# Kernel tuning notes

Measured on AMD Instinct MI355X. Metric: run time of the kernel, lower is better.

Reference implementation:

```python
import jax, jax.numpy as jnp
import numpy as np
from jax import lax

BN_EPS = 1e-5


def _conv(x, w):
    # stride-1, VALID conv; the torch 'locally connected' layer shares weights
    # across pixels, so it is exactly a standard conv2d.
    return lax.conv_general_dilated(
        x, w, window_strides=(1, 1), padding='VALID',
        dimension_numbers=('NCHW', 'OIHW', 'NCHW'))


def _batchnorm(x, gamma, beta):
    # training-mode BatchNorm2d: batch statistics over (N, H, W)
    mean = jnp.mean(x, axis=(0, 2, 3), keepdims=True)
    var = jnp.var(x, axis=(0, 2, 3), keepdims=True)
    xhat = (x - mean) * lax.rsqrt(var + BN_EPS)
    return xhat * gamma[None, :, None, None] + beta[None, :, None, None]


def setup_inputs() -> dict:
    key = jax.random.key(0)
    ks = jax.random.split(key, 6)
    B = 16384
    x = jax.random.normal(ks[0], (B, 256), dtype=jnp.float32)
    w1 = jax.random.normal(ks[1], (16, 1, 3, 3), dtype=jnp.float32)
    w2 = jax.random.normal(ks[2], (32, 16, 2, 2), dtype=jnp.float32)
    w3 = jax.random.normal(ks[3], (64, 32, 1, 1), dtype=jnp.float32)
    fan_in = 64 * 13 * 13
    bound = 1.0 / np.sqrt(fan_in)
    fc_w = jax.random.uniform(ks[4], (10, fan_in), minval=-bound, maxval=bound, dtype=jnp.float32)
    fc_b = jax.random.uniform(ks[5], (10,), minval=-bound, maxval=bound, dtype=jnp.float32)
    return {
        'x': x, 'w1': w1, 'w2': w2, 'w3': w3,
        'g1': jnp.ones((16,), jnp.float32), 'b1': jnp.zeros((16,), jnp.float32),
        'g2': jnp.ones((32,), jnp.float32), 'b2': jnp.zeros((32,), jnp.float32),
        'g3': jnp.ones((64,), jnp.float32), 'b3': jnp.zeros((64,), jnp.float32),
        'fc_w': fc_w, 'fc_b': fc_b,
    }


def reference(x, w1, w2, w3, g1, b1, g2, b2, g3, b3, fc_w, fc_b):
    h = x.reshape(-1, 1, 16, 16)                     # [B,1,16,16]
    h = jax.nn.relu(_batchnorm(_conv(h, w1), g1, b1))  # [B,16,14,14]
    h = jax.nn.relu(_batchnorm(_conv(h, w2), g2, b2))  # [B,32,13,13]
    h = jax.nn.relu(_batchnorm(_conv(h, w3), g3, b3))  # [B,64,13,13]
    h = h.reshape(h.shape[0], -1)                    # [B, 64*13*13]
    # dropout is identity in eval/deterministic mode
    return h @ fc_w.T + fc_b                         # [B,10]
```

## Files before the change

### kernel.cpp

```cpp
#include <hip/hip_runtime.h>


#define NPART 1024
#define P2_OFF 32768
#define ST_OFF 229376
#define ST1 ST_OFF
#define ST2 (ST_OFF + 32)
#define ST3 (ST_OFF + 96)
#define C2R_OFF 230400
#define C1R_OFF 231424
#define C2P_OFF 262144
#define A2G_BYTE 5242880ull
#define FCB_N (13 * 8192)
#define A1S 24
#define A1B 384
#define A3P 1048

typedef __attribute__((ext_vector_type(8))) short bf16x8;
typedef __attribute__((ext_vector_type(4))) float f32x4;

__device__ __forceinline__ unsigned int f2bf(float f) {
  unsigned int u = __float_as_uint(f);
  return (u + 0x7fffu + ((u >> 16) & 1u)) >> 16;
}
__device__ __forceinline__ unsigned int pkbf(float a, float b) {
  unsigned ua = __float_as_uint(a) + 0x8000u;
  unsigned ub = __float_as_uint(b) + 0x8000u;
  return __builtin_amdgcn_perm(ub, ua, 0x07060302u);
}
__device__ __forceinline__ short cvtbf(float a) {
  return (short)((__float_as_uint(a) + 0x8000u) >> 16);
}

__device__ __forceinline__ void conv1_mfma(
    const float* __restrict__ sxi,
    short* ph_buf,
    int r, int b, int q, bf16x8 a1f, f32x4 c1i)
{
  bf16x8 bf = {0, 0, 0, 0, 0, 0, 0, 0};
  unsigned* bu = (unsigned*)&bf;
  if (q == 0) {
    bu[0] = pkbf(sxi[r * 16 + b],           sxi[r * 16 + b + 1]);
    bu[1] = pkbf(sxi[r * 16 + b + 2],       sxi[(r + 1) * 16 + b]);
    bu[2] = pkbf(sxi[(r + 1) * 16 + b + 1], sxi[(r + 1) * 16 + b + 2]);
    bu[3] = pkbf(sxi[(r + 2) * 16 + b],     sxi[(r + 2) * 16 + b + 1]);
  } else if (q == 1) {
    bu[0] = pkbf(sxi[(r + 2) * 16 + b + 2], 0.f);
  }
  f32x4 acc = c1i;
  acc = __builtin_amdgcn_mfma_f32_16x16x32_bf16(a1f, bf, acc, 0, 0, 0);
  float v0 = acc[0] > 0.f ? acc[0] : 0.f;
  float v1 = acc[1] > 0.f ? acc[1] : 0.f;
  float v2 = acc[2] > 0.f ? acc[2] : 0.f;
  float v3 = acc[3] > 0.f ? acc[3] : 0.f;
  uint2 pk;
  pk.x = pkbf(v0, v1);
  pk.y = pkbf(v2, v3);
  *(uint2*)(ph_buf + (r & 1) * A1B + b * A1S + 4 * q) = pk;
}

__device__ __forceinline__ bf16x8 conv1_afrag(const float* w1, float rs1b,
                                              int b, int q) {
  bf16x8 v;
#pragma unroll
  for (int j = 0; j < 8; ++j) {
    int tap = 8 * q + j;
    v[j] = (tap < 9) ? (short)f2bf(w1[b * 9 + tap] * rs1b) : (short)0;
  }
  return v;
}

__global__ __launch_bounds__(256) void k1_xsyrk(
    const float* __restrict__ x, float* __restrict__ parts)
{
  __shared__ float sx[16 * 256];
  const int tid = threadIdx.x, w = tid >> 6, lane = tid & 63;
  const int b = lane & 15, q = lane >> 4;
  {
    const float4* xs = (const float4*)(x + (size_t)blockIdx.x * (16 * 256));
    float4* sd = (float4*)sx;
    for (int e = tid; e < 16 * 64; e += 256) sd[e] = xs[e];
  }
  __syncthreads();
  const int di = (b < 9) ? (b / 3) : 0;
  const int dj = (b < 9) ? (b - di * 3) : 0;
  const int h = q >> 1, jb = (q & 1) * 8;
  f32x4 acc = {0.f, 0.f, 0.f, 0.f};
#pragma unroll 1
  for (int t = 0; t < 4; ++t) {
    const float* sxi = sx + (w * 4 + t) * 256;
#pragma unroll 1
    for (int s = 0; s < 7; ++s) {
      bf16x8 af;
      unsigned* au = (unsigned*)&af;
      if (b < 9) {
        const float* srow = sxi + (2 * s + h + di) * 16 + dj;
#pragma unroll
        for (int cc = 0; cc < 4; ++cc) {
          float v0 = (jb + 2 * cc     < 14) ? srow[jb + 2 * cc]     : 0.f;
          float v1 = (jb + 2 * cc + 1 < 14) ? srow[jb + 2 * cc + 1] : 0.f;
          au[cc] = pkbf(v0, v1);
        }
      } else if (b == 9) {
#pragma unroll
        for (int cc = 0; cc < 4; ++cc) {
          unsigned lo = (jb + 2 * cc     < 14) ? 0x3F80u : 0u;
          unsigned hi = (jb + 2 * cc + 1 < 14) ? 0x3F800000u : 0u;
          au[cc] = lo | hi;
        }
      } else {
#pragma unroll
        for (int cc = 0; cc < 4; ++cc) au[cc] = 0u;
      }
      acc = __builtin_amdgcn_mfma_f32_16x16x32_bf16(af, af, acc, 0, 0, 0);
    }
  }
  __syncthreads();
  float* redc = sx;
#pragma unroll
  for (int rr = 0; rr < 4; ++rr)
    redc[w * 256 + (4 * q + rr) * 16 + b] = acc[rr];
  __syncthreads();
  parts[blockIdx.x * 256 + tid] =
      redc[tid] + redc[256 + tid] + redc[512 + tid] + redc[768 + tid];
}

__global__ __launch_bounds__(256) void k_stats1a(
    const float* __restrict__ parts, float* __restrict__ ws)
{
  const int e = blockIdx.x, tid = threadIdx.x;
  const int w = tid >> 6, lane = tid & 63;
  __shared__ float rs[4];
  float s = 0.f;
#pragma unroll 4
  for (int i = tid; i < 1024; i += 256) s += parts[i * 256 + e];
#pragma unroll
  for (int d = 1; d < 64; d <<= 1) s += __shfl_xor(s, d);
  if (lane == 0) rs[w] = s;
  __syncthreads();
  if (tid == 0) ws[C1R_OFF + e] = rs[0] + rs[1] + rs[2] + rs[3];
}

__global__ __launch_bounds__(64) void k_stats1b(
    const float* __restrict__ w1, const float* __restrict__ gamma,
    const float* __restrict__ beta, float* __restrict__ ws)
{
  const int c = threadIdx.x;
  if (c >= 16) return;
  const float* C = ws + C1R_OFF;
  float wr[9];
#pragma unroll
  for (int p = 0; p < 9; ++p) wr[p] = w1[c * 9 + p];
  float msum = 0.f;
#pragma unroll
  for (int p = 0; p < 9; ++p) msum += wr[p] * C[9 * 16 + p];
  float e2 = 0.f;
#pragma unroll
  for (int a = 0; a < 9; ++a)
#pragma unroll
    for (int bb = 0; bb < 9; ++bb)
      e2 += wr[a] * wr[bb] * C[a * 16 + bb];
  const float inv_n = 1.0f / (16384.0f * 196.0f);
  float mean = msum * inv_n;
  float var  = e2 * inv_n - mean * mean;
  float sv   = gamma[c] * rsqrtf(var + 1e-5f);
  ws[ST1 + c]      = sv;
  ws[ST1 + 16 + c] = beta[c] - mean * sv;
}

__global__ __launch_bounds__(256) void k_stats2(
    const float* __restrict__ gamma, const float* __restrict__ beta,
    float* __restrict__ ws, int nch, int part_off, int st_off, float inv_n)
{
  const int c = blockIdx.x, tid = threadIdx.x;
  const int w = tid >> 6, lane = tid & 63;
  __shared__ float rs[4], rq[4];
  float s = 0.f, q = 0.f;
#pragma unroll 4
  for (int i = tid; i < NPART; i += 256) {
    s += ws[part_off + i * 2 * nch + c];
    q += ws[part_off + i * 2 * nch + nch + c];
  }
#pragma unroll
  for (int d = 1; d < 64; d <<= 1) {
    s += __shfl_xor(s, d);
    q += __shfl_xor(q, d);
  }
  if (lane == 0) { rs[w] = s; rq[w] = q; }
  __syncthreads();
  if (tid == 0) {
    float st = rs[0] + rs[1] + rs[2] + rs[3];
    float qt = rq[0] + rq[1] + rq[2] + rq[3];
    float mean = st * inv_n;
    float var  = qt * inv_n - mean * mean;
    float sv   = gamma[c] * rsqrtf(var + 1e-5f);
    ws[st_off + c]       = sv;
    ws[st_off + nch + c] = beta[c] - mean * sv;
  }
}

__global__ __launch_bounds__(256) void k3_conv2_stats(
    const float* __restrict__ x, const float* __restrict__ w1,
    const float* __restrict__ w2, float* __restrict__ ws)
{
  __shared__ float sx_s[16 * 256 + 16];
  __shared__ alignas(16) short a1h[4 * 2 * A1B];
  __shared__ float redf[256];
  const int tid = threadIdx.x, w = tid >> 6, lane = tid & 63;
  const int b = lane & 15, q = lane >> 4;
  {
    const float4* xs = (const float4*)(x + (size_t)blockIdx.x * (16 * 256));
    float4* sd = (float4*)sx_s;
    for (int e = tid; e < 16 * 64; e += 256) sd[e] = xs[e];
    if (tid < 16) sx_s[16 * 256 + tid] = 0.f;
  }
  bf16x8 a1f = conv1_afrag(w1, ws[ST1 + b], b, q);
  f32x4 c1i;
#pragma unroll
  for (int r = 0; r < 4; ++r) c1i[r] = ws[ST1 + 16 + 4 * q + r];
  bf16x8 b2h[4];
#pragma unroll
  for (int ks = 0; ks < 2; ++ks)
#pragma unroll
    for (int nt = 0; nt < 2; ++nt) {
      bf16x8 vh;
#pragma unroll
      for (int j = 0; j < 8; ++j) {
        int kk = 8 * (q & 1) + j, dj = q >> 1;
        vh[j] = (short)f2bf(w2[(nt * 16 + b) * 64 + kk * 4 + ks * 2 + dj]);
      }
      b2h[ks * 2 + nt] = vh;
    }
  const float vb = (b < 13) ? 1.f : 0.f;
  const int colAr = (b + (q >> 1) < 15) ? (b + (q >> 1)) : 15;
  const int offAl = colAr * A1S + 8 * (q & 1);
  __syncthreads();

  float s2r[2][4] = {{0.f,0.f,0.f,0.f},{0.f,0.f,0.f,0.f}};
  float q2r[2][4] = {{0.f,0.f,0.f,0.f},{0.f,0.f,0.f,0.f}};
  short* ph = a1h + w * (2 * A1B);
#pragma unroll 1
  for (int t = 0; t < 4; ++t) {
    const float* sxi = sx_s + (w * 4 + t) * 256;
    conv1_mfma(sxi, ph, 0, b, q, a1f, c1i);
    __builtin_amdgcn_wave_barrier();
#pragma unroll 1
    for (int i = 0; i < 13; ++i) {
      conv1_mfma(sxi, ph, i + 1, b, q, a1f, c1i);
      __builtin_amdgcn_wave_barrier();
      bf16x8 ah0 = *(const bf16x8*)(ph + (i & 1) * A1B + offAl);
      bf16x8 ah1 = *(const bf16x8*)(ph + ((i + 1) & 1) * A1B + offAl);
      f32x4 acc2[2] = {{0.f,0.f,0.f,0.f},{0.f,0.f,0.f,0.f}};
#pragma unroll
      for (int nt = 0; nt < 2; ++nt) {
        acc2[nt] = __builtin_amdgcn_mfma_f32_16x16x32_bf16(b2h[nt], ah0, acc2[nt], 0, 0, 0);
        acc2[nt] = __builtin_amdgcn_mfma_f32_16x16x32_bf16(b2h[2 + nt], ah1, acc2[nt], 0, 0, 0);
      }
#pragma unroll
      for (int nt = 0; nt < 2; ++nt)
#pragma unroll
        for (int r = 0; r < 4; ++r) {
          float ym = acc2[nt][r] * vb;
          s2r[nt][r] += ym;
          q2r[nt][r] = fmaf(ym, acc2[nt][r], q2r[nt][r]);
        }
      __builtin_amdgcn_wave_barrier();
    }
  }
#pragma unroll
  for (int nt = 0; nt < 2; ++nt)
#pragma unroll
    for (int r = 0; r < 4; ++r) {
      float sv = s2r[nt][r], qv = q2r[nt][r];
      sv += __shfl_xor(sv, 1); sv += __shfl_xor(sv, 2);
      sv += __shfl_xor(sv, 4); sv += __shfl_xor(sv, 8);
      qv += __shfl_xor(qv, 1); qv += __shfl_xor(qv, 2);
      qv += __shfl_xor(qv, 4); qv += __shfl_xor(qv, 8);
      if (b == 0) {
        redf[w * 64 + nt * 16 + 4 * q + r]      = sv;
        redf[w * 64 + 32 + nt * 16 + 4 * q + r] = qv;
      }
    }
  __syncthreads();
  if (tid < 64)
    ws[P2_OFF + blockIdx.x * 64 + tid] =
        redf[tid] + redf[64 + tid] + redf[128 + tid] + redf[192 + tid];
}

__global__ __launch_bounds__(256) void k5_a2(
    const float* __restrict__ x, const float* __restrict__ w1,
    const float* __restrict__ w2, float* __restrict__ ws,
    short* __restrict__ a2g, float* __restrict__ parts)
{
  __shared__ float sx_s[16 * 256 + 16];
  __shared__ alignas(16) short a1h[4 * 2 * A1B];
  __shared__ alignas(16) short xt4[4 * 32 * 40];
  __shared__ float s2red[4 * 32];
  const int tid = threadIdx.x, w = tid >> 6, lane = tid & 63;
  const int b = lane & 15, q = lane >> 4;
  {
    const float4* xs = (const float4*)(x + (size_t)blockIdx.x * (16 * 256));
    float4* sd = (float4*)sx_s;
    for (int e = tid; e < 16 * 64; e += 256) sd[e] = xs[e];
    if (tid < 16) sx_s[16 * 256 + tid] = 0.f;
  }
  bf16x8 a1f = conv1_afrag(w1, ws[ST1 + b], b, q);
  f32x4 c1i;
#pragma unroll
  for (int r = 0; r < 4; ++r) c1i[r] = ws[ST1 + 16 + 4 * q + r];
  bf16x8 b2h[4];
#pragma unroll
  for (int ks = 0; ks < 2; ++ks)
#pragma unroll
    for (int nt = 0; nt < 2; ++nt) {
      float rs2b = ws[ST2 + nt * 16 + b];
      bf16x8 vh;
#pragma unroll
      for (int j = 0; j < 8; ++j) {
        int kk = 8 * (q & 1) + j, dj = q >> 1;
        vh[j] = (short)f2bf(w2[(nt * 16 + b) * 64 + kk * 4 + ks * 2 + dj] * rs2b);
      }
      b2h[ks * 2 + nt] = vh;
    }
  f32x4 c2i[2];
#pragma unroll
  for (int nt = 0; nt < 2; ++nt)
#pragma unroll
    for (int r = 0; r < 4; ++r)
      c2i[nt][r] = (b < 13) ? ws[ST2 + 32 + nt * 16 + 4 * q + r] : -1e30f;
  const int colAr = (b + (q >> 1) < 15) ? (b + (q >> 1)) : 15;
  const int offAl = colAr * A1S + 8 * (q & 1);
  short* xt = xt4 + w * 1280;
  __syncthreads();

  f32x4 accT0 = {0.f,0.f,0.f,0.f}, accT1 = {0.f,0.f,0.f,0.f},
        accT2 = {0.f,0.f,0.f,0.f};
  float s2aR[2][4] = {{0.f,0.f,0.f,0.f},{0.f,0.f,0.f,0.f}};
  short* ph = a1h + w * (2 * A1B);
#pragma unroll 1
  for (int t = 0; t < 4; ++t) {
    const int img = blockIdx.x * 16 + w * 4 + t;
    const float* sxi = sx_s + (w * 4 + t) * 256;
    conv1_mfma(sxi, ph, 0, b, q, a1f, c1i);
    __builtin_amdgcn_wave_barrier();
#pragma unroll 1
    for (int i = 0; i < 13; ++i) {
      conv1_mfma(sxi, ph, i + 1, b, q, a1f, c1i);
      __builtin_amdgcn_wave_barrier();
      bf16x8 ah0 = *(const bf16x8*)(ph + (i & 1) * A1B + offAl);
      bf16x8 ah1 = *(const bf16x8*)(ph + ((i + 1) & 1) * A1B + offAl);
#pragma unroll
      for (int nt = 0; nt < 2; ++nt) {
        f32x4 acc2 = c2i[nt];
        acc2 = __builtin_amdgcn_mfma_f32_16x16x32_bf16(b2h[nt], ah0, acc2, 0, 0, 0);
        acc2 = __builtin_amdgcn_mfma_f32_16x16x32_bf16(b2h[2 + nt], ah1, acc2, 0, 0, 0);
        float vm[4];
#pragma unroll
        for (int r = 0; r < 4; ++r) {
          vm[r] = acc2[r] > 0.f ? acc2[r] : 0.f;
          s2aR[nt][r] += vm[r];
          xt[(nt * 16 + 4 * q + r) * 40 + (i & 1) * 16 + b] = cvtbf(vm[r]);
        }
        if (b < 13) {
          uint2 pk;
          pk.x = pkbf(vm[0], vm[1]);
          pk.y = pkbf(vm[2], vm[3]);
          *(uint2*)(a2g + (size_t)img * 5408 + (size_t)(i * 13 + b) * 32 +
                    nt * 16 + 4 * q) = pk;
        }
      }
      __builtin_amdgcn_wave_barrier();
      if (i & 1) {
        bf16x8 xf0 = *(const bf16x8*)(xt + b * 40 + 8 * q);
        bf16x8 xf1 = *(const bf16x8*)(xt + (16 + b) * 40 + 8 * q);
        accT0 = __builtin_amdgcn_mfma_f32_16x16x32_bf16(xf0, xf0, accT0, 0, 0, 0);
        accT1 = __builtin_amdgcn_mfma_f32_16x16x32_bf16(xf0, xf1, accT1, 0, 0, 0);
        accT2 = __builtin_amdgcn_mfma_f32_16x16x32_bf16(xf1, xf1, accT2, 0, 0, 0);
      }
      __builtin_amdgcn_wave_barrier();
    }
    {
      uint2 z; z.x = 0u; z.y = 0u;
      *(uint2*)(xt + b * 40 + 16 + 4 * q) = z;
      *(uint2*)(xt + (16 + b) * 40 + 16 + 4 * q) = z;
      __builtin_amdgcn_wave_barrier();
      bf16x8 xf0 = *(const bf16x8*)(xt + b * 40 + 8 * q);
      bf16x8 xf1 = *(const bf16x8*)(xt + (16 + b) * 40 + 8 * q);
      accT0 = __builtin_amdgcn_mfma_f32_16x16x32_bf16(xf0, xf0, accT0, 0, 0, 0);
      accT1 = __builtin_amdgcn_mfma_f32_16x16x32_bf16(xf0, xf1, accT1, 0, 0, 0);
      accT2 = __builtin_amdgcn_mfma_f32_16x16x32_bf16(xf1, xf1, accT2, 0, 0, 0);
      __builtin_amdgcn_wave_barrier();
    }
  }
#pragma unroll
  for (int nt = 0; nt < 2; ++nt)
#pragma unroll
    for (int r = 0; r < 4; ++r) {
      float sv = s2aR[nt][r];
      sv += __shfl_xor(sv, 1); sv += __shfl_xor(sv, 2);
      sv += __shfl_xor(sv, 4); sv += __shfl_xor(sv, 8);
      if (b == 0) s2red[w * 32 + nt * 16 + 4 * q + r] = sv;
    }
  float* redc = sx_s;
#pragma unroll
  for (int rr = 0; rr < 4; ++rr) {
    int m = 4 * q + rr;
    redc[w * 1024 + 0   + m * 16 + b] = accT0[rr];
    redc[w * 1024 + 256 + m * 16 + b] = accT1[rr];
    redc[w * 1024 + 512 + m * 16 + b] = accT2[rr];
  }
  __syncthreads();
  for (int e = tid; e < 768; e += 256)
    parts[blockIdx.x * 800 + e] =
        redc[e] + redc[1024 + e] + redc[2048 + e] + redc[3072 + e];
  if (tid < 32)
    parts[blockIdx.x * 800 + 768 + tid] =
        s2red[tid] + s2red[32 + tid] + s2red[64 + tid] + s2red[96 + tid];
}

__global__ __launch_bounds__(256) void k_statsC(
    const float* __restrict__ parts, float* __restrict__ ws)
{
  const int e = blockIdx.x, tid = threadIdx.x;
  const int w = tid >> 6, lane = tid & 63;
  __shared__ float rs[4];
  float s = 0.f;
#pragma unroll 4
  for (int i = tid; i < 1024; i += 256) s += parts[i * 800 + e];
#pragma unroll
  for (int d = 1; d < 64; d <<= 1) s += __shfl_xor(s, d);
  if (lane == 0) rs[w] = s;
  __syncthreads();
  if (tid == 0) ws[C2R_OFF + e] = rs[0] + rs[1] + rs[2] + rs[3];
}

__global__ __launch_bounds__(64) void k_stats3n(
    const float* __restrict__ w3, const float* __restrict__ gamma,
    const float* __restrict__ beta, float* __restrict__ ws)
{
  const int c3 = threadIdx.x;
  if (c3 >= 64) return;
  const float* C2R = ws + C2R_OFF;
  float wr[32];
#pragma unroll
  for (int k = 0; k < 32; ++k) wr[k] = w3[c3 * 32 + k];
  const float inv_n = 1.0f / (16384.0f * 169.0f);
  float msum = 0.f;
#pragma unroll
  for (int k = 0; k < 32; ++k) msum += wr[k] * C2R[768 + k];
  float e2 = 0.f;
  for (int a = 0; a < 16; ++a)
#pragma unroll
    for (int bb = 0; bb < 16; ++bb) {
      e2 += wr[a] * wr[bb] * C2R[a * 16 + bb];
      e2 += wr[16 + a] * wr[16 + bb] * C2R[512 + a * 16 + bb];
      e2 += 2.f * wr[a] * wr[16 + bb] * C2R[256 + a * 16 + bb];
    }
  float mean = msum * inv_n;
  float var  = e2 * inv_n - mean * mean;
  float sv   = gamma[c3] * rsqrtf(var + 1e-5f);
  ws[ST3 + c3]      = sv;
  ws[ST3 + 64 + c3] = beta[c3] - mean * sv;
}

__global__ __launch_bounds__(256) void k0_fcB(
    const float* __restrict__ fcw, unsigned int* __restrict__ fcB)
{
  int F = blockIdx.x * 256 + threadIdx.x;
  if (F >= FCB_N) return;
  int u = F & 3, q = (F >> 2) & 3, jj = (F >> 4) & 15;
  int mm = (F >> 8) & 31, i = F >> 13;
  int k0 = mm * 32 + q * 8 + u * 2;
  unsigned lo = 0, hi = 0;
  if (jj < 10) {
    int c0 = k0 >> 4, j0 = k0 & 15;
    if (j0 < 13) lo = f2bf(fcw[jj * 10816 + c0 * 169 + i * 13 + j0]);
    int c1 = (k0 + 1) >> 4, j1 = (k0 + 1) & 15;
    if (j1 < 13) hi = f2bf(fcw[jj * 10816 + c1 * 169 + i * 13 + j1]);
  }
  fcB[F] = lo | (hi << 16);
}

__global__ __launch_bounds__(256) void k7_fc(
    const short* __restrict__ a2g, const float* __restrict__ w3,
    const float* __restrict__ fcb, const float* __restrict__ ws,
    float* __restrict__ out)
{
  __shared__ alignas(16) short a3buf[16 * A3P];
  const int tid = threadIdx.x, w = tid >> 6, lane = tid & 63;
  const int b = lane & 15, q = lane >> 4;
  bf16x8 b3h[4];
  f32x4 c3i[4];
#pragma unroll
  for (int nt = 0; nt < 4; ++nt) {
    float s3 = ws[ST3 + nt * 16 + b];
    float t3 = ws[ST3 + 64 + nt * 16 + b];
    bf16x8 vh;
#pragma unroll
    for (int j = 0; j < 8; ++j)
      vh[j] = (short)f2bf(w3[(nt * 16 + b) * 32 + 8 * q + j] * s3);
    b3h[nt] = vh;
    c3i[nt][0] = t3;
#pragma unroll
    for (int r = 1; r < 4; ++r)
      c3i[nt][r] = (q < 3) ? t3 : -1e30f;
  }
  const bf16x8* fcB = (const bf16x8*)ws;
  f32x4 accF = {0.f, 0.f, 0.f, 0.f};
  const int pixc = (b < 12) ? b : 12;
  size_t ib[4];
#pragma unroll
  for (int t = 0; t < 4; ++t)
    ib[t] = (size_t)(blockIdx.x * 16 + w * 4 + t) * 5408;
  bf16x8 a2pre[4];
#pragma unroll
  for (int t = 0; t < 4; ++t)
    a2pre[t] = *(const bf16x8*)(a2g + ib[t] + pixc * 32 + 8 * q);

#pragma unroll 1
  for (int i = 0; i < 13; ++i) {
    bf16x8 a2cur[4];
#pragma unroll
    for (int t = 0; t < 4; ++t) a2cur[t] = a2pre[t];
    if (i < 12) {
#pragma unroll
      for (int t = 0; t < 4; ++t)
        a2pre[t] = *(const bf16x8*)(a2g + ib[t] +
                                    (size_t)((i + 1) * 13 + pixc) * 32 + 8 * q);
    }
#pragma unroll
    for (int t = 0; t < 4; ++t) {
      const int g = w * 4 + t;
#pragma unroll
      for (int nt = 0; nt < 4; ++nt) {
        f32x4 acc3 = c3i[nt];
        acc3 = __builtin_amdgcn_mfma_f32_16x16x32_bf16(a2cur[t], b3h[nt], acc3, 0, 0, 0);
        float v0 = acc3[0] > 0.f ? acc3[0] : 0.f;
        float v1 = acc3[1] > 0.f ? acc3[1] : 0.f;
        float v2 = acc3[2] > 0.f ? acc3[2] : 0.f;
        float v3 = acc3[3] > 0.f ? acc3[3] : 0.f;
        uint2 pk2;
        pk2.x = pkbf(v0, v1);
        pk2.y = pkbf(v2, v3);
        *(uint2*)(a3buf + g * A3P + (nt * 16 + b) * 16 + 4 * q) = pk2;
      }
    }
    __syncthreads();
#pragma unroll
    for (int mm = 0; mm < 8; ++mm) {
      bf16x8 af = *(const bf16x8*)(a3buf + b * A3P + w * 256 + mm * 32 + 8 * q);
      bf16x8 bw = fcB[((i * 32 + w * 8 + mm) * 16 + b) * 4 + q];
      accF = __builtin_amdgcn_mfma_f32_16x16x32_bf16(af, bw, accF, 0, 0, 0);
    }
    __syncthreads();
  }

  float* redf7 = (float*)a3buf;
#pragma unroll
  for (int r = 0; r < 4; ++r)
    redf7[w * 256 + (4 * q + r) * 16 + b] = accF[r];
  __syncthreads();
  if (tid < 160) {
    int img = tid / 10, jj = tid - img * 10;
    float s = redf7[img * 16 + jj] + redf7[256 + img * 16 + jj] +
              redf7[512 + img * 16 + jj] + redf7[768 + img * 16 + jj];
    out[(blockIdx.x * 16 + img) * 10 + jj] = s + fcb[jj];
  }
}

extern "C" void kernel_launch(void* const* d_in, const int* in_sizes, int n_in,
                              void* d_out, int out_size, void* d_ws, size_t ws_size,
                              hipStream_t stream) {
  (void)in_sizes; (void)n_in; (void)out_size; (void)ws_size;
  const float* x   = (const float*)d_in[0];
  const float* w1  = (const float*)d_in[1];
  const float* w2  = (const float*)d_in[2];
  const float* w3  = (const float*)d_in[3];
  const float* g1  = (const float*)d_in[4];
  const float* b1  = (const float*)d_in[5];
  const float* g2  = (const float*)d_in[6];
  const float* b2  = (const float*)d_in[7];
  const float* g3  = (const float*)d_in[8];
  const float* b3  = (const float*)d_in[9];
  const float* fcw = (const float*)d_in[10];
  const float* fcb = (const float*)d_in[11];
  float* out = (float*)d_out;
  float* ws  = (float*)d_ws;
  short* a2g = (short*)((char*)d_ws + A2G_BYTE);
  float* parts = ws + C2P_OFF;

  k1_xsyrk<<<1024, 256, 0, stream>>>(x, parts);
  k_stats1a<<<256, 256, 0, stream>>>(parts, ws);
  k_stats1b<<<1, 64, 0, stream>>>(w1, g1, b1, ws);
  k3_conv2_stats<<<1024, 256, 0, stream>>>(x, w1, w2, ws);
  k_stats2<<<32, 256, 0, stream>>>(g2, b2, ws, 32, P2_OFF, ST2,
                                   1.0f / (16384.0f * 169.0f));
  k5_a2<<<1024, 256, 0, stream>>>(x, w1, w2, ws, a2g, parts);
  k_statsC<<<800, 256, 0, stream>>>(parts, ws);
  k_stats3n<<<1, 64, 0, stream>>>(w3, g3, b3, ws);
  k0_fcB<<<FCB_N / 256, 256, 0, stream>>>(fcw, (unsigned int*)ws);
  k7_fc<<<1024, 256, 0, stream>>>(a2g, w3, fcb, ws, out);
}
```

Baseline: 278.9 us.

## Fuse BN stats reductions into producer kernels via atomics and last-block finalize

Replaces the per-block partial-sum buffers and the separate reduction/finalize kernels (stats1a/1b, stats2, statsC, stats3n) with float atomicAdd accumulation into a small workspace region. A completion counter lets the last block of each producer kernel compute the BN scale/shift. The fcB prep kernel is moved first and also zeroes the accumulators and counters. This drops five launches and the partial-buffer traffic, at the cost of atomic contention on a few hundred addresses and nondeterministic float summation order.

```diff
diff --git a/kernel.cpp b/kernel.cpp
--- a/kernel.cpp
+++ b/kernel.cpp
@@ -1,15 +1,16 @@
 #include <hip/hip_runtime.h>
 
 
-#define NPART 1024
-#define P2_OFF 32768
 #define ST_OFF 229376
 #define ST1 ST_OFF
 #define ST2 (ST_OFF + 32)
 #define ST3 (ST_OFF + 96)
-#define C2R_OFF 230400
-#define C1R_OFF 231424
-#define C2P_OFF 262144
+#define ACC1 114688
+#define ACC2 115200
+#define ACC3 115968
+#define CNT_OFF 118784
+#define ZB 114688
+#define ZN 4112
 #define A2G_BYTE 5242880ull
 #define FCB_N (13 * 8192)
 #define A1S 24
@@ -30,6 +31,9 @@
 }
 __device__ __forceinline__ short cvtbf(float a) {
   return (short)((__float_as_uint(a) + 0x8000u) >> 16);
+}
+__device__ __forceinline__ float aload(const float* p) {
+  return __hip_atomic_load(p, __ATOMIC_RELAXED, __HIP_MEMORY_SCOPE_AGENT);
 }
 
 __device__ __forceinline__ void conv1_mfma(
@@ -70,10 +74,32 @@
   return v;
 }
 
+__global__ __launch_bounds__(256) void k0_fcB(
+    const float* __restrict__ fcw, unsigned int* __restrict__ fcB)
+{
+  int F = blockIdx.x * 256 + threadIdx.x;
+  if (F >= FCB_N) return;
+  if (F < ZN) fcB[ZB + F] = 0u;
+  int u = F & 3, q = (F >> 2) & 3, jj = (F >> 4) & 15;
+  int mm = (F >> 8) & 31, i = F >> 13;
+  int k0 = mm * 32 + q * 8 + u * 2;
+  unsigned lo = 0, hi = 0;
+  if (jj < 10) {
+    int c0 = k0 >> 4, j0 = k0 & 15;
+    if (j0 < 13) lo = f2bf(fcw[jj * 10816 + c0 * 169 + i * 13 + j0]);
+    int c1 = (k0 + 1) >> 4, j1 = (k0 + 1) & 15;
+    if (j1 < 13) hi = f2bf(fcw[jj * 10816 + c1 * 169 + i * 13 + j1]);
+  }
+  fcB[F] = lo | (hi << 16);
+}
+
 __global__ __launch_bounds__(256) void k1_xsyrk(
-    const float* __restrict__ x, float* __restrict__ parts)
+    const float* __restrict__ x, const float* __restrict__ w1,
+    const float* __restrict__ gamma, const float* __restrict__ beta,
+    float* __restrict__ ws)
 {
   __shared__ float sx[16 * 256];
+  __shared__ bool islast;
   const int tid = threadIdx.x, w = tid >> 6, lane = tid & 63;
   const int b = lane & 15, q = lane >> 4;
   {
@@ -121,91 +147,49 @@
   for (int rr = 0; rr < 4; ++rr)
     redc[w * 256 + (4 * q + rr) * 16 + b] = acc[rr];
   __syncthreads();
-  parts[blockIdx.x * 256 + tid] =
-      redc[tid] + redc[256 + tid] + redc[512 + tid] + redc[768 + tid];
-}
-
-__global__ __launch_bounds__(256) void k_stats1a(
-    const float* __restrict__ parts, float* __restrict__ ws)
-{
-  const int e = blockIdx.x, tid = threadIdx.x;
-  const int w = tid >> 6, lane = tid & 63;
-  __shared__ float rs[4];
-  float s = 0.f;
-#pragma unroll 4
-  for (int i = tid; i < 1024; i += 256) s += parts[i * 256 + e];
-#pragma unroll
-  for (int d = 1; d < 64; d <<= 1) s += __shfl_xor(s, d);
-  if (lane == 0) rs[w] = s;
-  __syncthreads();
-  if (tid == 0) ws[C1R_OFF + e] = rs[0] + rs[1] + rs[2] + rs[3];
-}
-
-__global__ __launch_bounds__(64) void k_stats1b(
-    const float* __restrict__ w1, const float* __restrict__ gamma,
-    const float* __restrict__ beta, float* __restrict__ ws)
-{
-  const int c = threadIdx.x;
-  if (c >= 16) return;
-  const float* C = ws + C1R_OFF;
-  float wr[9];
-#pragma unroll
-  for (int p = 0; p < 9; ++p) wr[p] = w1[c * 9 + p];
-  float msum = 0.f;
-#pragma unroll
-  for (int p = 0; p < 9; ++p) msum += wr[p] * C[9 * 16 + p];
-  float e2 = 0.f;
-#pragma unroll
-  for (int a = 0; a < 9; ++a)
-#pragma unroll
-    for (int bb = 0; bb < 9; ++bb)
-      e2 += wr[a] * wr[bb] * C[a * 16 + bb];
-  const float inv_n = 1.0f / (16384.0f * 196.0f);
-  float mean = msum * inv_n;
-  float var  = e2 * inv_n - mean * mean;
-  float sv   = gamma[c] * rsqrtf(var + 1e-5f);
-  ws[ST1 + c]      = sv;
-  ws[ST1 + 16 + c] = beta[c] - mean * sv;
-}
-
-__global__ __launch_bounds__(256) void k_stats2(
-    const float* __restrict__ gamma, const float* __restrict__ beta,
-    float* __restrict__ ws, int nch, int part_off, int st_off, float inv_n)
-{
-  const int c = blockIdx.x, tid = threadIdx.x;
-  const int w = tid >> 6, lane = tid & 63;
-  __shared__ float rs[4], rq[4];
-  float s = 0.f, q = 0.f;
-#pragma unroll 4
-  for (int i = tid; i < NPART; i += 256) {
-    s += ws[part_off + i * 2 * nch + c];
-    q += ws[part_off + i * 2 * nch + nch + c];
-  }
-#pragma unroll
-  for (int d = 1; d < 64; d <<= 1) {
-    s += __shfl_xor(s, d);
-    q += __shfl_xor(q, d);
-  }
-  if (lane == 0) { rs[w] = s; rq[w] = q; }
+  atomicAdd(&ws[ACC1 + tid],
+            redc[tid] + redc[256 + tid] + redc[512 + tid] + redc[768 + tid]);
+  __threadfence();
   __syncthreads();
   if (tid == 0) {
-    float st = rs[0] + rs[1] + rs[2] + rs[3];
-    float qt = rq[0] + rq[1] + rq[2] + rq[3];
-    float mean = st * inv_n;
-    float var  = qt * inv_n - mean * mean;
-    float sv   = gamma[c] * rsqrtf(var + 1e-5f);
-    ws[st_off + c]       = sv;
-    ws[st_off + nch + c] = beta[c] - mean * sv;
+    unsigned old = atomicAdd((unsigned*)(ws + CNT_OFF) + 0, 1u);
+    islast = (old == 1023u);
+  }
+  __syncthreads();
+  if (!islast) return;
+  redc[tid] = aload(ws + ACC1 + tid);
+  __syncthreads();
+  if (tid < 16) {
+    float wr[9];
+#pragma unroll
+    for (int p = 0; p < 9; ++p) wr[p] = w1[tid * 9 + p];
+    float msum = 0.f;
+#pragma unroll
+    for (int p = 0; p < 9; ++p) msum += wr[p] * redc[9 * 16 + p];
+    float e2 = 0.f;
+#pragma unroll
+    for (int a = 0; a < 9; ++a)
+#pragma unroll
+      for (int bb = 0; bb < 9; ++bb)
+        e2 += wr[a] * wr[bb] * redc[a * 16 + bb];
+    const float inv_n = 1.0f / (16384.0f * 196.0f);
+    float mean = msum * inv_n;
+    float var  = e2 * inv_n - mean * mean;
+    float sv   = gamma[tid] * rsqrtf(var + 1e-5f);
+    ws[ST1 + tid]      = sv;
+    ws[ST1 + 16 + tid] = beta[tid] - mean * sv;
   }
 }
 
 __global__ __launch_bounds__(256) void k3_conv2_stats(
     const float* __restrict__ x, const float* __restrict__ w1,
-    const float* __restrict__ w2, float* __restrict__ ws)
+    const float* __restrict__ w2, const float* __restrict__ gamma,
+    const float* __restrict__ beta, float* __restrict__ ws)
 {
   __shared__ float sx_s[16 * 256 + 16];
   __shared__ alignas(16) short a1h[4 * 2 * A1B];
   __shared__ float redf[256];
+  __shared__ bool islast;
   const int tid = threadIdx.x, w = tid >> 6, lane = tid & 63;
   const int b = lane & 15, q = lane >> 4;
   {
@@ -283,19 +267,39 @@
     }
   __syncthreads();
   if (tid < 64)
-    ws[P2_OFF + blockIdx.x * 64 + tid] =
-        redf[tid] + redf[64 + tid] + redf[128 + tid] + redf[192 + tid];
+    atomicAdd(&ws[ACC2 + tid],
+              redf[tid] + redf[64 + tid] + redf[128 + tid] + redf[192 + tid]);
+  __threadfence();
+  __syncthreads();
+  if (tid == 0) {
+    unsigned old = atomicAdd((unsigned*)(ws + CNT_OFF) + 1, 1u);
+    islast = (old == 1023u);
+  }
+  __syncthreads();
+  if (!islast) return;
+  if (tid < 64) redf[tid] = aload(ws + ACC2 + tid);
+  __syncthreads();
+  if (tid < 32) {
+    const float inv_n = 1.0f / (16384.0f * 169.0f);
+    float mean = redf[tid] * inv_n;
+    float var  = redf[32 + tid] * inv_n - mean * mean;
+    float sv   = gamma[tid] * rsqrtf(var + 1e-5f);
+    ws[ST2 + tid]      = sv;
+    ws[ST2 + 32 + tid] = beta[tid] - mean * sv;
+  }
 }
 
 __global__ __launch_bounds__(256) void k5_a2(
     const float* __restrict__ x, const float* __restrict__ w1,
-    const float* __restrict__ w2, float* __restrict__ ws,
-    short* __restrict__ a2g, float* __restrict__ parts)
+    const float* __restrict__ w2, const float* __restrict__ w3,
+    const float* __restrict__ gamma, const float* __restrict__ beta,
+    float* __restrict__ ws, short* __restrict__ a2g)
 {
   __shared__ float sx_s[16 * 256 + 16];
   __shared__ alignas(16) short a1h[4 * 2 * A1B];
   __shared__ alignas(16) short xt4[4 * 32 * 40];
   __shared__ float s2red[4 * 32];
+  __shared__ bool islast;
   const int tid = threadIdx.x, w = tid >> 6, lane = tid & 63;
   const int b = lane & 15, q = lane >> 4;
   {
@@ -411,74 +415,53 @@
   }
   __syncthreads();
   for (int e = tid; e < 768; e += 256)
-    parts[blockIdx.x * 800 + e] =
-        redc[e] + redc[1024 + e] + redc[2048 + e] + redc[3072 + e];
+    atomicAdd(&ws[ACC3 + e],
+              redc[e] + redc[1024 + e] + redc[2048 + e] + redc[3072 + e]);
   if (tid < 32)
-    parts[blockIdx.x * 800 + 768 + tid] =
-        s2red[tid] + s2red[32 + tid] + s2red[64 + tid] + s2red[96 + tid];
-}
-
-__global__ __launch_bounds__(256) void k_statsC(
-    const float* __restrict__ parts, float* __restrict__ ws)
-{
-  const int e = blockIdx.x, tid = threadIdx.x;
-  const int w = tid >> 6, lane = tid & 63;
-  __shared__ float rs[4];
-  float s = 0.f;
-#pragma unroll 4
-  for (int i = tid; i < 1024; i += 256) s += parts[i * 800 + e];
-#pragma unroll
-  for (int d = 1; d < 64; d <<= 1) s += __shfl_xor(s, d);
-  if (lane == 0) rs[w] = s;
-  __syncthreads();
-  if (tid == 0) ws[C2R_OFF + e] = rs[0] + rs[1] + rs[2] + rs[3];
-}
-
-__global__ __launch_bounds__(64) void k_stats3n(
-    const float* __restrict__ w3, const float* __restrict__ gamma,
-    const float* __restrict__ beta, float* __restrict__ ws)
-{
-  const int c3 = threadIdx.x;
-  if (c3 >= 64) return;
-  const float* C2R = ws + C2R_OFF;
-  float wr[32];
-#pragma unroll
-  for (int k = 0; k < 32; ++k) wr[k] = w3[c3 * 32 + k];
-  const float inv_n = 1.0f / (16384.0f * 169.0f);
-  float msum = 0.f;
-#pragma unroll
-  for (int k = 0; k < 32; ++k) msum += wr[k] * C2R[768 + k];
-  float e2 = 0.f;
-  for (int a = 0; a < 16; ++a)
-#pragma unroll
-    for (int bb = 0; bb < 16; ++bb) {
-      e2 += wr[a] * wr[bb] * C2R[a * 16 + bb];
-      e2 += wr[16 + a] * wr[16 + bb] * C2R[512 + a * 16 + bb];
-      e2 += 2.f * wr[a] * wr[16 + bb] * C2R[256 + a * 16 + bb];
-    }
-  float mean = msum * inv_n;
-  float var  = e2 * inv_n - mean * mean;
-  float sv   = gamma[c3] * rsqrtf(var + 1e-5f);
-  ws[ST3 + c3]      = sv;
-  ws[ST3 + 64 + c3] = beta[c3] - mean * sv;
-}
-
-__global__ __launch_bounds__(256) void k0_fcB(
-    const float* __restrict__ fcw, unsigned int* __restrict__ fcB)
-{
-  int F = blockIdx.x * 256 + threadIdx.x;
-  if (F >= FCB_N) return;
-  int u = F & 3, q = (F >> 2) & 3, jj = (F >> 4) & 15;
-  int mm = (F >> 8) & 31, i = F >> 13;
-  int k0 = mm * 32 + q * 8 + u * 2;
-  unsigned lo = 0, hi = 0;
-  if (jj < 10) {
-    int c0 = k0 >> 4, j0 = k0 & 15;
-    if (j0 < 13) lo = f2bf(fcw[jj * 10816 + c0 * 169 + i * 13 + j0]);
-    int c1 = (k0 + 1) >> 4, j1 = (k0 + 1) & 15;
-    if (j1 < 13) hi = f2bf(fcw[jj * 10816 + c1 * 169 + i * 13 + j1]);
-  }
-  fcB[F] = lo | (hi << 16);
+    atomicAdd(&ws[ACC3 + 768 + tid],
+              s2red[tid] + s2red[32 + tid] + s2red[64 + tid] + s2red[96 + tid]);
+  __threadfence();
+  __syncthreads();
+  if (tid == 0) {
+    unsigned old = atomicAdd((unsigned*)(ws + CNT_OFF) + 2, 1u);
+    islast = (old == 1023u);
+  }
+  __syncthreads();
+  if (!islast) return;
+  for (int e = tid; e < 800; e += 256) redc[e] = aload(ws + ACC3 + e);
+  __syncthreads();
+  {
+    const int c3 = tid & 63, seg = tid >> 6;
+    float wr[32];
+#pragma unroll
+    for (int k = 0; k < 32; ++k) wr[k] = w3[c3 * 32 + k];
+    float e2p = 0.f;
+    for (int a = seg * 4; a < seg * 4 + 4; ++a)
+#pragma unroll
+      for (int bb = 0; bb < 16; ++bb) {
+        e2p += wr[a] * wr[bb] * redc[a * 16 + bb];
+        e2p += wr[16 + a] * wr[16 + bb] * redc[512 + a * 16 + bb];
+        e2p += 2.f * wr[a] * wr[16 + bb] * redc[256 + a * 16 + bb];
+      }
+    float msum = 0.f;
+    if (seg == 0) {
+#pragma unroll
+      for (int k = 0; k < 32; ++k) msum += wr[k] * redc[768 + k];
+    }
+    redc[1024 + seg * 64 + c3] = e2p;
+    if (seg == 0) redc[1280 + c3] = msum;
+  }
+  __syncthreads();
+  if (tid < 64) {
+    const float inv_n = 1.0f / (16384.0f * 169.0f);
+    float e2 = redc[1024 + tid] + redc[1088 + tid] +
+               redc[1152 + tid] + redc[1216 + tid];
+    float mean = redc[1280 + tid] * inv_n;
+    float var  = e2 * inv_n - mean * mean;
+    float sv   = gamma[tid] * rsqrtf(var + 1e-5f);
+    ws[ST3 + tid]      = sv;
+    ws[ST3 + 64 + tid] = beta[tid] - mean * sv;
+  }
 }
 
 __global__ __launch_bounds__(256) void k7_fc(
@@ -587,17 +570,10 @@
   float* out = (float*)d_out;
   float* ws  = (float*)d_ws;
   short* a2g = (short*)((char*)d_ws + A2G_BYTE);
-  float* parts = ws + C2P_OFF;
-
-  k1_xsyrk<<<1024, 256, 0, stream>>>(x, parts);
-  k_stats1a<<<256, 256, 0, stream>>>(parts, ws);
-  k_stats1b<<<1, 64, 0, stream>>>(w1, g1, b1, ws);
-  k3_conv2_stats<<<1024, 256, 0, stream>>>(x, w1, w2, ws);
-  k_stats2<<<32, 256, 0, stream>>>(g2, b2, ws, 32, P2_OFF, ST2,
-                                   1.0f / (16384.0f * 169.0f));
-  k5_a2<<<1024, 256, 0, stream>>>(x, w1, w2, ws, a2g, parts);
-  k_statsC<<<800, 256, 0, stream>>>(parts, ws);
-  k_stats3n<<<1, 64, 0, stream>>>(w3, g3, b3, ws);
+
   k0_fcB<<<FCB_N / 256, 256, 0, stream>>>(fcw, (unsigned int*)ws);
+  k1_xsyrk<<<1024, 256, 0, stream>>>(x, w1, g1, b1, ws);
+  k3_conv2_stats<<<1024, 256, 0, stream>>>(x, w1, w2, g2, b2, ws);
+  k5_a2<<<1024, 256, 0, stream>>>(x, w1, w2, w3, g3, b3, ws, a2g);
   k7_fc<<<1024, 256, 0, stream>>>(a2g, w3, fcb, ws, out);
 }
```

After: 480.9 us. 72.4% more time.
